# Kernel optimization log

Hardware: AMD Instinct MI355X
Metric: run time of the kernel (lower is better)

## Reference

```python
import jax, jax.numpy as jnp
import numpy as np

N = 4096          # residues (2 chains x 2048)
CHAINS = 2
LMAX = 2
L = (LMAX + 1) ** 2            # 9 spherical coefficients
BBC = 32                       # bb_channels
NBB = 3                        # n_bb_atoms - 1
SPH = BBC + NBB                # 35 sphere channels fed to attention
KNN = 20
LRK = 40
HEADS = 8
HC = 32
VC = HC // 4                   # attn_value_channels = 8
EDGE_F = 32                    # 16 RBF + 16 positional
L_IDX = np.repeat(np.arange(LMAX + 1), 2 * np.arange(LMAX + 1) + 1)  # degree of each of the 9 coeffs


def so3_linear(x, w, b):
    # x: [N,L,Cin]; w: [LMAX+1,Cin,Cout] shared across m within each degree l; bias only on l=0
    out = jnp.einsum('nlc,lcd->nld', x, w[L_IDX])
    return out.at[:, 0, :].add(b)


def _rbf(d):
    mu = jnp.linspace(0.0, 20.0, 16)
    sigma = 20.0 / 16
    return jnp.exp(-(((d[..., None] - mu) / sigma) ** 2))


def _edge_pos_embed(src, dst):
    d = (src - dst).astype(jnp.float32)
    freq = jnp.exp(jnp.arange(0, 16, 2, dtype=jnp.float32) * (-np.log(10000.0) / 16))
    ang = d[:, None] * freq
    return jnp.concatenate([jnp.cos(ang), jnp.sin(ang)], axis=-1)


def setup_inputs():
    key = jax.random.key(0)
    ks = jax.random.split(key, 16)
    n = lambda i, shp, s=1.0: jax.random.normal(ks[i], shp) * s
    return {
        'X_ca': n(0, (N, 3), 10.0),
        'bb_rel': n(1, (N, NBB, 3)),
        'bb_features': n(2, (N, L, BBC)),
        'batch': jnp.repeat(jnp.arange(CHAINS), N // CHAINS),
        'x_mask': jax.random.uniform(ks[3], (N,)) < 0.02,
        'noising_mask': jax.random.uniform(ks[4], (N,)) < 0.5,
        'attn_w1': n(5, (2 * SPH + EDGE_F, HC), 0.05), 'attn_b1': jnp.zeros((HC,)),
        'attn_w2': n(6, (HC, HEADS), 0.05), 'attn_b2': jnp.zeros((HEADS,)),
        'wv': n(7, (LMAX + 1, SPH, HEADS * VC), 0.05), 'bv': jnp.zeros((HEADS * VC,)),
        'wo': n(8, (LMAX + 1, HEADS * VC, BBC), 0.05), 'bo': jnp.zeros((BBC,)),
        'wg': n(9, (BBC, BBC), 0.05), 'bg': jnp.zeros((BBC,)),
        'wf': n(10, (LMAX + 1, BBC, BBC), 0.05), 'bf': jnp.zeros((BBC,)),
        'w_xca': n(11, (LMAX + 1, BBC, 1), 0.05), 'b_xca': jnp.zeros((1,)),
        'w_gate': n(12, (BBC, 1), 0.05), 'b_gate': jnp.zeros((1,)),
        'w_bb': n(13, (LMAX + 1, BBC, NBB), 0.05), 'b_bb': jnp.zeros((NBB,)),
    }


def reference(X_ca, bb_rel, bb_features, batch, x_mask, noising_mask,
              attn_w1, attn_b1, attn_w2, attn_b2, wv, bv, wo, bo, wg, bg, wf, bf,
              w_xca, b_xca, w_gate, b_gate, w_bb, b_bb):
    Nn = X_ca.shape[0]
    BIG = jnp.float32(1e30)
    # ---- graph construction (knn_graph + sample_inv_cubic_edges) ----
    x2 = jnp.sum(X_ca * X_ca, axis=-1)
    D2 = jnp.maximum(x2[:, None] + x2[None, :] - 2.0 * (X_ca @ X_ca.T), 0.0)  # [N,N]
    same = batch[:, None] == batch[None, :]
    eye = jnp.eye(Nn, dtype=bool)
    mask_pair = x_mask[:, None] | x_mask[None, :]
    invalid = (~same) | eye | mask_pair
    knn_idx = jax.lax.top_k(-jnp.where(invalid, BIG, D2), KNN)[1]   # [N,KNN] sources per target
    # long-range: inverse-cubic distance weights, Gumbel top-k sampling, excluding knn picks
    logits = jnp.where(invalid, -BIG, -1.5 * jnp.log(D2 + 1e-6))
    rows = jnp.arange(Nn)[:, None]
    logits = logits.at[rows, knn_idx].set(-BIG)
    gumb = jax.random.gumbel(jax.random.key(1), (Nn, Nn))
    lr_idx = jax.lax.top_k(logits + gumb, LRK)[1]                   # [N,LRK]
    src = jnp.concatenate([knn_idx.reshape(-1), lr_idx.reshape(-1)])
    dst = jnp.concatenate([jnp.repeat(jnp.arange(Nn), KNN), jnp.repeat(jnp.arange(Nn), LRK)])
    # ---- edge features: RBF(dist) + relative positional embedding ----
    dvec = X_ca[src] - X_ca[dst]
    dist = jnp.linalg.norm(dvec, axis=-1)
    edge_feat = jnp.concatenate([_rbf(dist), _edge_pos_embed(src, dst)], axis=-1)  # [M,32]
    # ---- assemble SO3 node embedding [N,L,35] ----
    node = jnp.zeros((Nn, L, SPH), X_ca.dtype)
    node = node.at[:, :, :BBC].set(bb_features)
    node = node.at[:, 1:4, BBC:].set(jnp.swapaxes(bb_rel, -1, -2))  # l=1 coeffs carry bb_rel
    node = node.at[:, 0, SPH - 1].set(noising_mask.astype(X_ca.dtype))
    # ---- equivariant graph attention (simplified TransBlockV2) ----
    inv = node[:, 0, :]                                             # invariant (l=0) features
    a_in = jnp.concatenate([inv[src], inv[dst], edge_feat], axis=-1)
    h = jax.nn.silu(a_in @ attn_w1 + attn_b1)
    logit = h @ attn_w2 + attn_b2                                   # [M,HEADS]
    mx = jax.ops.segment_max(logit, dst, num_segments=Nn)
    p = jnp.exp(logit - mx[dst])
    Z = jax.ops.segment_sum(p, dst, num_segments=Nn)
    alpha = p / (Z[dst] + 1e-9)                                     # segment softmax per target/head
    v = so3_linear(node, wv, bv)[src].reshape(-1, L, HEADS, VC)     # gather source values
    msg = (v * alpha[:, None, :, None]).reshape(-1, L, HEADS * VC)
    agg = jax.ops.segment_sum(msg, dst, num_segments=Nn)            # scatter to targets
    out = so3_linear(agg, wo, bo)                                   # [N,L,32]
    gate = jax.nn.silu(out[:, 0, :] @ wg + bg)                      # invariant-gated FFN
    out = out + so3_linear(out, wf, bf) * gate[:, None, :]
    # ---- coordinate / backbone updates ----
    upd_x = so3_linear(out, w_xca, b_xca)                           # [N,L,1]
    vec = upd_x[:, 1:4, 0]                                          # l=1 -> 3-vector
    g2 = jax.nn.softplus(out[:, 0, :] @ w_gate + b_gate)            # [N,1]
    new_X = X_ca + jnp.where(noising_mask[:, None], vec * g2, 0.0)
    upd_bb = so3_linear(out, w_bb, b_bb)                            # [N,L,3]
    dbb = jnp.swapaxes(upd_bb[:, 1:4, :], -1, -2)                   # [N,3,3]
    new_bb = bb_rel + jnp.where(noising_mask[:, None, None], dbb, 0.0)
    return new_X, new_bb, out
```

## Files before the change

### kernel.cpp

```cpp
#include <hip/hip_runtime.h>
#include <hip/hip_bf16.h>
#include <stdint.h>

#define NN 4096
#define CS 2048
#define KNN 20
#define LRK 40
#define EPN 60
#define NE (NN*EPN)
#define SPHC 35
#define BBCC 32
#define NHEAD 8
#define HVD 64
#define HCD 32
#define LT 9
#define MAXC 384
#define VMB ((NN*LT)/4)
#define NPB (NN/8)

#define INVAL_D2 0xFFFFFFFEu
#define CONSUMED 0xFFFFFFFFu

__device__ __forceinline__ float bf2f(__hip_bfloat16 x) { return __bfloat162float(x); }
__device__ __forceinline__ float bflo(uint32_t d) { return __uint_as_float(d << 16); }
__device__ __forceinline__ float bfhi(uint32_t d) { return __uint_as_float(d & 0xFFFF0000u); }

__device__ __forceinline__ float fast_exp(float x) {
  return __builtin_amdgcn_exp2f(x * 1.4426950408889634f);
}
__device__ __forceinline__ float fast_cos(float a) {
  float rev = a * 0.15915494309189535f;
  rev = rev - __builtin_rintf(rev);
  return __builtin_amdgcn_cosf(rev);
}
__device__ __forceinline__ float fast_sin(float a) {
  float rev = a * 0.15915494309189535f;
  rev = rev - __builtin_rintf(rev);
  return __builtin_amdgcn_sinf(rev);
}

__device__ __forceinline__ float neglogu_f(int i, int j) {
  uint32_t c = ((uint32_t)(i & 2047) << 12) | (uint32_t)j;
  const uint32_t ks0 = 0u, ks1 = 1u, ks2 = 0x1BD11BDBu;
  uint32_t x0 = c + ks0;
  uint32_t x1 = (c + 0x800000u) + ks1;
#define TF_R(r) { x0 += x1; x1 = (x1 << (r)) | (x1 >> (32 - (r))); x1 ^= x0; }
  TF_R(13) TF_R(15) TF_R(26) TF_R(6)   x0 += ks1; x1 += ks2 + 1u;
  TF_R(17) TF_R(29) TF_R(16) TF_R(24)  x0 += ks2; x1 += ks0 + 2u;
  TF_R(13) TF_R(15) TF_R(26) TF_R(6)   x0 += ks0; x1 += ks1 + 3u;
  TF_R(17) TF_R(29) TF_R(16) TF_R(24)  x0 += ks1; x1 += ks2 + 4u;
  TF_R(13) TF_R(15) TF_R(26) TF_R(6)   x0 += ks2; x1 += ks0 + 5u;
#undef TF_R
  uint32_t b = (i >= 2048) ? x1 : x0;
  float u = __uint_as_float((b >> 9) | 0x3F800000u) - 1.0f;
  u = u + 1.17549435e-38f;
  return -logf(u);
}

__global__ __launch_bounds__(256) void prep_proj_kernel(const float* __restrict__ X,
                                                        const int* __restrict__ batch,
                                                        const int* __restrict__ xmask,
                                                        const int* __restrict__ nmask,
                                                        const float* __restrict__ bbf,
                                                        const float* __restrict__ w1,
                                                        const float* __restrict__ b1,
                                                        float4* __restrict__ Xw,
                                                        uint32_t* __restrict__ bm,
                                                        float* __restrict__ Pn,
                                                        float* __restrict__ Pd) {
#pragma clang fp contract(off)
  int tid = threadIdx.x;
  if (blockIdx.x < NPB) {
    int t = tid & 31;
    int n = blockIdx.x * 8 + (tid >> 5);
    float bv_ = bbf[(size_t)n * (LT*BBCC) + t];
    float an = 0.f, ad = b1[t];
    #pragma unroll 8
    for (int c = 0; c < BBCC; c++) {
      float bc = __shfl(bv_, (tid & 32) + c, 64);
      an = fmaf(bc, w1[c * HCD + t], an);
      ad = fmaf(bc, w1[(SPHC + c) * HCD + t], ad);
    }
    float nm = nmask[n] ? 1.f : 0.f;
    an = fmaf(nm, w1[34 * HCD + t], an);
    ad = fmaf(nm, w1[69 * HCD + t], ad);
    Pn[n * HCD + t] = an;
    Pd[n * HCD + t] = ad;
  } else {
    int n = (blockIdx.x - NPB) * 256 + tid;
    if (n >= NN) return;
    float x = X[n*3+0], y = X[n*3+1], z = X[n*3+2];
    float x2 = (x*x + y*y) + z*z;
    Xw[n] = make_float4(x, y, z, x2);
    bm[n] = ((uint32_t)batch[n] << 1) | (xmask[n] ? 1u : 0u);
  }
}

__device__ __forceinline__ void sel2l(uint32_t* val, uint32_t* hist2,
                                      uint32_t* candk, uint32_t* candp,
                                      uint32_t* sh, int* sel,
                                      int k, int base, int cb, int tid) {
  {
    uint4* h4 = (uint4*)hist2;
    uint4 z; z.x = 0; z.y = 0; z.z = 0; z.w = 0;
    h4[tid] = z; h4[tid + 256] = z;
  }
  if (tid == 0) { sh[2] = 0; sh[3] = 0; }
  __syncthreads();
  #pragma unroll
  for (int q = 0; q < 8; q++) {
    uint32_t key = val[tid + (q << 8)];
    atomicAdd(&hist2[key >> 21], 1u);
  }
  __syncthreads();
  uint32_t h[8], s = 0;
  #pragma unroll
  for (int q = 0; q < 8; q++) { h[q] = hist2[tid*8 + q]; s += h[q]; }
  uint32_t cum = s;
  #pragma unroll
  for (int off = 1; off < 64; off <<= 1) {
    uint32_t o = __shfl_up(cum, off, 64);
    if ((tid & 63) >= off) cum += o;
  }
  if ((tid & 63) == 63) sh[8 + (tid >> 6)] = cum;
  __syncthreads();
  uint32_t woff = 0;
  for (int w = 0; w < (tid >> 6); w++) woff += sh[8 + w];
  uint32_t cumAll = cum + woff;
  uint32_t cumBefore = cumAll - s;
  uint32_t rk = (uint32_t)k;
  if (rk > cumBefore && rk <= cumAll) {
    uint32_t rloc = rk - cumBefore, lp = 0;
    bool done = false;
    #pragma unroll
    for (int q = 0; q < 8; q++) {
      lp += h[q];
      if (!done && rloc <= lp) { sh[0] = (uint32_t)(tid*8 + q); sh[1] = rloc - (lp - h[q]); done = true; }
    }
  }
  __syncthreads();
  const uint32_t B = sh[0], r = sh[1];
  #pragma unroll
  for (int q = 0; q < 8; q++) {
    int pos = tid + (q << 8);
    uint32_t key = val[pos];
    if ((key >> 21) == B) {
      uint32_t idx = atomicAdd(&sh[2], 1u);
      if (idx < MAXC) { candk[idx] = key; candp[idx] = (uint32_t)pos; }
    }
  }
  __syncthreads();
  int m = (int)sh[2]; if (m > MAXC) m = MAXC;
  if (tid < 64) {
    for (int ci = tid; ci < m; ci += 64) {
      unsigned long long k64 = ((unsigned long long)candk[ci] << 32) | candp[ci];
      uint32_t rank = 0;
      for (int j = 0; j < m; j++) {
        unsigned long long o = ((unsigned long long)candk[j] << 32) | candp[j];
        rank += (o < k64) ? 1u : 0u;
      }
      if (rank == r - 1) { sh[0] = candk[ci]; sh[1] = candp[ci]; }
    }
  }
  __syncthreads();
  const uint32_t vstar = sh[0], istar = sh[1];
  #pragma unroll
  for (int q = 0; q < 8; q++) {
    int pos = tid + (q << 8);
    uint32_t key = val[pos];
    if (key < vstar || (key == vstar && (uint32_t)pos <= istar)) {
      uint32_t slot = atomicAdd(&sh[3], 1u);
      sel[base + (int)slot] = cb + pos;
    }
  }
  __syncthreads();
}

__global__ __launch_bounds__(256) void select_vmat_kernel(const float4* __restrict__ Xw,
                                                          const uint32_t* __restrict__ bm,
                                                          int* __restrict__ srcO,
                                                          const float* __restrict__ bbf,
                                                          const float* __restrict__ bbrel,
                                                          const int* __restrict__ nmask,
                                                          const float* __restrict__ wv,
                                                          const float* __restrict__ bv,
                                                          __hip_bfloat16* __restrict__ V) {
#pragma clang fp contract(off)
  const int tid = threadIdx.x;
  if (blockIdx.x >= NN) {
    int row = (blockIdx.x - NN) * 4 + (tid >> 6);
    int d = tid & 63;
    if (row >= NN * LT) return;
    int n = row / LT, l = row % LT;
    int li = (l == 0) ? 0 : (l < 4 ? 1 : 2);
    const float* w = wv + (size_t)li * SPHC * HVD;
    float acc = (l == 0) ? bv[d] : 0.f;
    const float* nb = bbf + (size_t)(n*LT + l) * BBCC;
    for (int c = 0; c < BBCC; c++) acc = fmaf(nb[c], w[c*HVD + d], acc);
    if (l >= 1 && l < 4) {
      for (int b = 0; b < 3; b++)
        acc = fmaf(bbrel[(size_t)(n*3 + b)*3 + (l-1)], w[(32+b)*HVD + d], acc);
    }
    if (l == 0) acc = fmaf(nmask[n] ? 1.f : 0.f, w[34*HVD + d], acc);
    V[(size_t)row * HVD + d] = __float2bfloat16(acc);
    return;
  }
  __shared__ uint32_t val[CS];
  __shared__ uint32_t hist2[2048];
  __shared__ uint32_t candk[MAXC];
  __shared__ uint32_t candp[MAXC];
  __shared__ uint32_t sh[12];
  __shared__ int sel[EPN];
  const int i = blockIdx.x;
  const uint32_t bmi = bm[i];

  if (bmi & 1u) {
    if (tid < KNN) srcO[(size_t)i * EPN + tid] = tid;
    else if (tid < EPN) srcO[(size_t)i * EPN + tid] = tid - KNN;
    return;
  }
  const int cb = (int)(bmi >> 1) * CS;
  const float4 xi = Xw[i];

  #pragma unroll
  for (int q = 0; q < 8; q++) {
    int pos = tid + (q << 8);
    int j = cb + pos;
    float4 xj = Xw[j];
    uint32_t bmj = bm[j];
    bool inval = ((bmj & 1u) != 0u) || (j == i);
    float dot = xi.x*xj.x + xi.y*xj.y + xi.z*xj.z;
    float d2r = (xi.w + xj.w) - 2.0f*dot;
    float d2 = d2r > 0.0f ? d2r : 0.0f;
    val[pos] = inval ? INVAL_D2 : __float_as_uint(d2);
  }
  __syncthreads();

  sel2l(val, hist2, candk, candp, sh, sel, KNN, 0, cb, tid);

  if (tid < KNN) val[sel[tid] - cb] = CONSUMED;
  __syncthreads();

  #pragma unroll
  for (int q = 0; q < 8; q++) {
    int pos = tid + (q << 8);
    uint32_t v = val[pos];
    uint32_t skey;
    if (v >= INVAL_D2) skey = CONSUMED;
    else {
      float d2p = __uint_as_float(v) + 1e-6f;
      float w = d2p * sqrtf(d2p) * neglogu_f(i, cb + pos);
      skey = __float_as_uint(w);
    }
    val[pos] = skey;
  }
  __syncthreads();

  sel2l(val, hist2, candk, candp, sh, sel, LRK, KNN, cb, tid);

  if (tid < EPN) srcO[(size_t)i * EPN + tid] = sel[tid];
}

__global__ __launch_bounds__(256) void edge_kernel(const int* __restrict__ src,
                                                   const float4* __restrict__ Xw,
                                                   const float* __restrict__ Pn,
                                                   const float* __restrict__ Pd,
                                                   const float* __restrict__ w1,
                                                   const float* __restrict__ w2,
                                                   const float* __restrict__ b2,
                                                   float* __restrict__ logitO) {
  const float FR[8] = {1.0f, 0.31622776601683794f, 0.1f, 0.031622776601683794f,
                       0.01f, 0.0031622776601683794f, 0.001f, 0.00031622776601683794f};
  __shared__ float w1cf[BBCC][HCD];
  __shared__ float w2f[HCD][NHEAD];
  __shared__ float b2f[NHEAD];
  __shared__ float ef[8][BBCC];
  __shared__ float hbuf[8][HCD];
  int tid = threadIdx.x;
  for (int q = tid; q < BBCC*HCD; q += 256) w1cf[q >> 5][q & 31] = w1[70*HCD + q];
  if (tid < HCD*NHEAD) w2f[tid >> 3][tid & 7] = w2[tid];
  if (tid < NHEAD) b2f[tid] = b2[tid];
  int sub = tid >> 5, t = tid & 31;
  int e = blockIdx.x * 8 + sub;
  int d = e / EPN;
  int s = src[e];
  float4 xs = Xw[s], xd = Xw[d];
  float dx = xs.x - xd.x, dy = xs.y - xd.y, dz = xs.z - xd.z;
  float dist = sqrtf(dx*dx + dy*dy + dz*dz);
  if (t < 16) {
    float mu = (20.0f / 15.0f) * (float)t;
    float zz = (dist - mu) / 1.25f;
    ef[sub][t] = fast_exp(-zz * zz);
  } else {
    int k = t - 16;
    float del = (float)(s - d);
    float a = del * FR[k & 7];
    ef[sub][t] = (k < 8) ? fast_cos(a) : fast_sin(a);
  }
  __syncthreads();
  float a = Pn[s * HCD + t] + Pd[d * HCD + t];
  #pragma unroll
  for (int k = 0; k < BBCC; k++) a = fmaf(ef[sub][k], w1cf[k][t], a);
  hbuf[sub][t] = a / (1.f + fast_exp(-a));
  __syncthreads();
  if (tid < 64) {
    int e2 = tid >> 3, hh = tid & 7;
    float lg = b2f[hh];
    #pragma unroll
    for (int c = 0; c < HCD; c++) lg = fmaf(hbuf[e2][c], w2f[c][hh], lg);
    logitO[(size_t)(blockIdx.x * 8 + e2) * NHEAD + hh] = lg;
  }
}

__global__ __launch_bounds__(256) void node_kernel(const int* __restrict__ src,
                                                  const float* __restrict__ logit,
                                                  const __hip_bfloat16* __restrict__ V,
                                                  const float* __restrict__ wo,
                                                  const float* __restrict__ bo,
                                                  const float* __restrict__ wg,
                                                  const float* __restrict__ bg,
                                                  const float* __restrict__ wf,
                                                  const float* __restrict__ bfb,
                                                  const float* __restrict__ w_xca,
                                                  const float* __restrict__ w_gate,
                                                  const float* __restrict__ b_gate,
                                                  const float* __restrict__ w_bb,
                                                  const float* __restrict__ X,
                                                  const float* __restrict__ bbrel,
                                                  const int* __restrict__ nmask,
                                                  float* __restrict__ out) {
  const int n = blockIdx.x, t = threadIdx.x;
  __shared__ float alpha[EPN][NHEAD];
  __shared__ int slist[EPN];
  __shared__ float aggp[4][LT][HVD];
  __shared__ float agg[LT][HVD];
  __shared__ float o0[LT][BBCC];
  __shared__ float ofin[LT][BBCC];
  __shared__ float gate[BBCC];
  if (t < EPN) slist[t] = src[(size_t)n * EPN + t];
  for (int idx = t; idx < EPN * NHEAD; idx += 256)
    alpha[idx >> 3][idx & 7] = logit[(size_t)n * 480 + idx];
  __syncthreads();
  if (t < NHEAD) {
    float m = -1e30f;
    for (int e = 0; e < EPN; e++) m = fmaxf(m, alpha[e][t]);
    float Z = 0.f;
    for (int e = 0; e < EPN; e++) { float p = expf(alpha[e][t] - m); alpha[e][t] = p; Z += p; }
    float iz = 1.f / (Z + 1e-9f);
    for (int e = 0; e < EPN; e++) alpha[e][t] *= iz;
  }
  __syncthreads();
  {
    const int wave = t >> 6, lane = t & 63;
    const int hM = lane & 7;
    const int hT = (lane & 31) >> 2;
    float accm[8];
    #pragma unroll
    for (int j = 0; j < 8; j++) accm[j] = 0.f;
    float acct0 = 0.f, acct1 = 0.f;
    const int e0 = wave * 15;
    #pragma unroll 5
    for (int e = e0; e < e0 + 15; e++) {
      const uint32_t* Vr = (const uint32_t*)(V + (size_t)slist[e] * (LT * HVD));
      uint4 m = ((const uint4*)Vr)[lane];
      uint32_t tl = (lane < 32) ? Vr[256 + lane] : 0u;
      float am = alpha[e][hM];
      float at = alpha[e][hT];
      accm[0] = fmaf(am, bflo(m.x), accm[0]);
      accm[1] = fmaf(am, bfhi(m.x), accm[1]);
      accm[2] = fmaf(am, bflo(m.y), accm[2]);
      accm[3] = fmaf(am, bfhi(m.y), accm[3]);
      accm[4] = fmaf(am, bflo(m.z), accm[4]);
      accm[5] = fmaf(am, bfhi(m.z), accm[5]);
      accm[6] = fmaf(am, bflo(m.w), accm[6]);
      accm[7] = fmaf(am, bfhi(m.w), accm[7]);
      acct0 = fmaf(at, bflo(tl), acct0);
      acct1 = fmaf(at, bfhi(tl), acct1);
    }
    const int l = lane >> 3, c0 = (lane & 7) * 8;
    #pragma unroll
    for (int j = 0; j < 8; j++) aggp[wave][l][c0 + j] = accm[j];
    if (lane < 32) {
      aggp[wave][8][2*lane]     = acct0;
      aggp[wave][8][2*lane + 1] = acct1;
    }
  }
  __syncthreads();
  for (int idx = t; idx < LT * HVD; idx += 256) {
    int l = idx >> 6, c = idx & 63;
    agg[l][c] = (aggp[0][l][c] + aggp[1][l][c]) + (aggp[2][l][c] + aggp[3][l][c]);
  }
  __syncthreads();
  for (int idx = t; idx < LT * BBCC; idx += 256) {
    int l = idx >> 5, d = idx & 31;
    int li = (l == 0) ? 0 : (l < 4 ? 1 : 2);
    float a = (l == 0) ? bo[d] : 0.f;
    const float* w = wo + (size_t)li * HVD * BBCC;
    for (int c = 0; c < HVD; c++) a = fmaf(agg[l][c], w[c * BBCC + d], a);
    o0[l][d] = a;
  }
  __syncthreads();
  if (t < BBCC) {
    float a = bg[t];
    for (int c = 0; c < BBCC; c++) a = fmaf(o0[0][c], wg[c * BBCC + t], a);
    gate[t] = a / (1.f + expf(-a));
  }
  __syncthreads();
  for (int idx = t; idx < LT * BBCC; idx += 256) {
    int l = idx >> 5, d = idx & 31;
    int li = (l == 0) ? 0 : (l < 4 ? 1 : 2);
    float a = (l == 0) ? bfb[d] : 0.f;
    const float* w = wf + (size_t)li * BBCC * BBCC;
    for (int c = 0; c < BBCC; c++) a = fmaf(o0[l][c], w[c * BBCC + d], a);
    float r = o0[l][d] + a * gate[d];
    ofin[l][d] = r;
    out[49152 + (size_t)n * 288 + idx] = r;
  }
  __syncthreads();
  if (t < 16) {
    float a2 = b_gate[0];
    for (int c = 0; c < BBCC; c++) a2 = fmaf(ofin[0][c], w_gate[c], a2);
    float g2 = fmaxf(a2, 0.f) + log1pf(expf(-fabsf(a2)));
    bool noise = nmask[n] != 0;
    if (t < 3) {
      float a = 0.f;
      for (int d2 = 0; d2 < BBCC; d2++) a = fmaf(ofin[1 + t][d2], w_xca[32 + d2], a);
      float nx = X[n * 3 + t] + (noise ? a * g2 : 0.f);
      out[(size_t)n * 3 + t] = nx;
    }
    if (t < 9) {
      int b = t / 3, c = t % 3;
      float a = 0.f;
      for (int d2 = 0; d2 < BBCC; d2++) a = fmaf(ofin[1 + c][d2], w_bb[(32 + d2) * 3 + b], a);
      float nb = bbrel[(size_t)(n * 3 + b) * 3 + c] + (noise ? a : 0.f);
      out[12288 + (size_t)n * 9 + b * 3 + c] = nb;
    }
  }
}

extern "C" void kernel_launch(void* const* d_in, const int* in_sizes, int n_in,
                              void* d_out, int out_size, void* d_ws, size_t ws_size,
                              hipStream_t stream) {
  (void)in_sizes; (void)n_in; (void)out_size;
  const float* X      = (const float*)d_in[0];
  const float* bbrel  = (const float*)d_in[1];
  const float* bbf    = (const float*)d_in[2];
  const int* batch    = (const int*)d_in[3];
  const int* xmask    = (const int*)d_in[4];
  const int* nmask    = (const int*)d_in[5];
  const float* w1     = (const float*)d_in[6];
  const float* b1     = (const float*)d_in[7];
  const float* w2     = (const float*)d_in[8];
  const float* b2     = (const float*)d_in[9];
  const float* wv     = (const float*)d_in[10];
  const float* bv     = (const float*)d_in[11];
  const float* wo     = (const float*)d_in[12];
  const float* bo     = (const float*)d_in[13];
  const float* wg     = (const float*)d_in[14];
  const float* bg     = (const float*)d_in[15];
  const float* wf     = (const float*)d_in[16];
  const float* bfb    = (const float*)d_in[17];
  const float* w_xca  = (const float*)d_in[18];
  const float* w_gate = (const float*)d_in[20];
  const float* b_gate = (const float*)d_in[21];
  const float* w_bb   = (const float*)d_in[22];

  if (ws_size < 18939904) return;
  char* ws = (char*)d_ws;
  uint32_t* bmp   = (uint32_t*)(ws + 0);
  int*      srcl  = (int*)(ws + 16384);
  float*    logit = (float*)(ws + 999424);
  __hip_bfloat16* V = (__hip_bfloat16*)(ws + 8863744);
  float*    Pn    = (float*)(ws + 13582336);
  float*    Pd    = (float*)(ws + 14106624);
  float4*   Xw    = (float4*)(ws + 14630912);
  float*    out   = (float*)d_out;

  prep_proj_kernel<<<NPB + 16, 256, 0, stream>>>(X, batch, xmask, nmask, bbf, w1, b1,
                                                 Xw, bmp, Pn, Pd);
  select_vmat_kernel<<<NN + VMB, 256, 0, stream>>>(Xw, bmp, srcl, bbf, bbrel, nmask,
                                                   wv, bv, V);
  edge_kernel<<<NE / 8, 256, 0, stream>>>(srcl, Xw, Pn, Pd, w1, w2, b2, logit);
  node_kernel<<<NN, 256, 0, stream>>>(srcl, logit, V, wo, bo, wg, bg, wf, bfb,
                                      w_xca, w_gate, b_gate, w_bb, X, bbrel, nmask, out);
}
```

Before: 273.3 us.

## Fuse edge logit computation into node kernel and merge prep into graph kernel

Four launches become two. Edge MLP logits are now computed per target node inside node_kernel, with edge features passed through wave shuffles, so the logit buffer is no longer written to and read back from global memory. The prep work (Pn/Pd projection, plus the Xw/bm packing) is folded into the selection/V kernel, and coordinates and masks are read directly from the inputs. The trade-off is a longer serial edge phase in each node block (8 iterations, some with idle half-waves) and per-edge data now recomputed per node.

```diff
diff --git a/kernel.cpp b/kernel.cpp
--- a/kernel.cpp
+++ b/kernel.cpp
@@ -7,7 +7,6 @@
 #define KNN 20
 #define LRK 40
 #define EPN 60
-#define NE (NN*EPN)
 #define SPHC 35
 #define BBCC 32
 #define NHEAD 8
@@ -21,7 +20,6 @@
 #define INVAL_D2 0xFFFFFFFEu
 #define CONSUMED 0xFFFFFFFFu
 
-__device__ __forceinline__ float bf2f(__hip_bfloat16 x) { return __bfloat162float(x); }
 __device__ __forceinline__ float bflo(uint32_t d) { return __uint_as_float(d << 16); }
 __device__ __forceinline__ float bfhi(uint32_t d) { return __uint_as_float(d & 0xFFFF0000u); }
 
@@ -57,45 +55,6 @@
   return -logf(u);
 }
 
-__global__ __launch_bounds__(256) void prep_proj_kernel(const float* __restrict__ X,
-                                                        const int* __restrict__ batch,
-                                                        const int* __restrict__ xmask,
-                                                        const int* __restrict__ nmask,
-                                                        const float* __restrict__ bbf,
-                                                        const float* __restrict__ w1,
-                                                        const float* __restrict__ b1,
-                                                        float4* __restrict__ Xw,
-                                                        uint32_t* __restrict__ bm,
-                                                        float* __restrict__ Pn,
-                                                        float* __restrict__ Pd) {
-#pragma clang fp contract(off)
-  int tid = threadIdx.x;
-  if (blockIdx.x < NPB) {
-    int t = tid & 31;
-    int n = blockIdx.x * 8 + (tid >> 5);
-    float bv_ = bbf[(size_t)n * (LT*BBCC) + t];
-    float an = 0.f, ad = b1[t];
-    #pragma unroll 8
-    for (int c = 0; c < BBCC; c++) {
-      float bc = __shfl(bv_, (tid & 32) + c, 64);
-      an = fmaf(bc, w1[c * HCD + t], an);
-      ad = fmaf(bc, w1[(SPHC + c) * HCD + t], ad);
-    }
-    float nm = nmask[n] ? 1.f : 0.f;
-    an = fmaf(nm, w1[34 * HCD + t], an);
-    ad = fmaf(nm, w1[69 * HCD + t], ad);
-    Pn[n * HCD + t] = an;
-    Pd[n * HCD + t] = ad;
-  } else {
-    int n = (blockIdx.x - NPB) * 256 + tid;
-    if (n >= NN) return;
-    float x = X[n*3+0], y = X[n*3+1], z = X[n*3+2];
-    float x2 = (x*x + y*y) + z*z;
-    Xw[n] = make_float4(x, y, z, x2);
-    bm[n] = ((uint32_t)batch[n] << 1) | (xmask[n] ? 1u : 0u);
-  }
-}
-
 __device__ __forceinline__ void sel2l(uint32_t* val, uint32_t* hist2,
                                       uint32_t* candk, uint32_t* candp,
                                       uint32_t* sh, int* sel,
@@ -176,21 +135,43 @@
   __syncthreads();
 }
 
-__global__ __launch_bounds__(256) void select_vmat_kernel(const float4* __restrict__ Xw,
-                                                          const uint32_t* __restrict__ bm,
-                                                          int* __restrict__ srcO,
-                                                          const float* __restrict__ bbf,
-                                                          const float* __restrict__ bbrel,
-                                                          const int* __restrict__ nmask,
-                                                          const float* __restrict__ wv,
-                                                          const float* __restrict__ bv,
-                                                          __hip_bfloat16* __restrict__ V) {
+__global__ __launch_bounds__(256) void graph_kernel(const float* __restrict__ X,
+                                                    const int* __restrict__ batch,
+                                                    const int* __restrict__ xmask,
+                                                    const int* __restrict__ nmask,
+                                                    const float* __restrict__ bbf,
+                                                    const float* __restrict__ bbrel,
+                                                    const float* __restrict__ wv,
+                                                    const float* __restrict__ bv,
+                                                    const float* __restrict__ w1,
+                                                    const float* __restrict__ b1,
+                                                    int* __restrict__ srcO,
+                                                    __hip_bfloat16* __restrict__ V,
+                                                    float* __restrict__ Pn,
+                                                    float* __restrict__ Pd) {
 #pragma clang fp contract(off)
   const int tid = threadIdx.x;
+  if (blockIdx.x >= NN + VMB) {
+    int t = tid & 31;
+    int n = (blockIdx.x - NN - VMB) * 8 + (tid >> 5);
+    float bv_ = bbf[(size_t)n * (LT*BBCC) + t];
+    float an = 0.f, ad = b1[t];
+    #pragma unroll 8
+    for (int c = 0; c < BBCC; c++) {
+      float bc = __shfl(bv_, (tid & 32) + c, 64);
+      an = fmaf(bc, w1[c * HCD + t], an);
+      ad = fmaf(bc, w1[(SPHC + c) * HCD + t], ad);
+    }
+    float nm = nmask[n] ? 1.f : 0.f;
+    an = fmaf(nm, w1[34 * HCD + t], an);
+    ad = fmaf(nm, w1[69 * HCD + t], ad);
+    Pn[n * HCD + t] = an;
+    Pd[n * HCD + t] = ad;
+    return;
+  }
   if (blockIdx.x >= NN) {
     int row = (blockIdx.x - NN) * 4 + (tid >> 6);
     int d = tid & 63;
-    if (row >= NN * LT) return;
     int n = row / LT, l = row % LT;
     int li = (l == 0) ? 0 : (l < 4 ? 1 : 2);
     const float* w = wv + (size_t)li * SPHC * HVD;
@@ -212,25 +193,25 @@
   __shared__ uint32_t sh[12];
   __shared__ int sel[EPN];
   const int i = blockIdx.x;
-  const uint32_t bmi = bm[i];
-
-  if (bmi & 1u) {
+
+  if (xmask[i]) {
     if (tid < KNN) srcO[(size_t)i * EPN + tid] = tid;
     else if (tid < EPN) srcO[(size_t)i * EPN + tid] = tid - KNN;
     return;
   }
-  const int cb = (int)(bmi >> 1) * CS;
-  const float4 xi = Xw[i];
+  const int cb = batch[i] * CS;
+  const float xi0 = X[i*3+0], xi1 = X[i*3+1], xi2 = X[i*3+2];
+  const float x2i = (xi0*xi0 + xi1*xi1) + xi2*xi2;
 
   #pragma unroll
   for (int q = 0; q < 8; q++) {
     int pos = tid + (q << 8);
     int j = cb + pos;
-    float4 xj = Xw[j];
-    uint32_t bmj = bm[j];
-    bool inval = ((bmj & 1u) != 0u) || (j == i);
-    float dot = xi.x*xj.x + xi.y*xj.y + xi.z*xj.z;
-    float d2r = (xi.w + xj.w) - 2.0f*dot;
+    float xj0 = X[j*3+0], xj1 = X[j*3+1], xj2 = X[j*3+2];
+    float x2j = (xj0*xj0 + xj1*xj1) + xj2*xj2;
+    bool inval = (xmask[j] != 0) || (j == i);
+    float dot = xi0*xj0 + xi1*xj1 + xi2*xj2;
+    float d2r = (x2i + x2j) - 2.0f*dot;
     float d2 = d2r > 0.0f ? d2r : 0.0f;
     val[pos] = inval ? INVAL_D2 : __float_as_uint(d2);
   }
@@ -261,60 +242,13 @@
   if (tid < EPN) srcO[(size_t)i * EPN + tid] = sel[tid];
 }
 
-__global__ __launch_bounds__(256) void edge_kernel(const int* __restrict__ src,
-                                                   const float4* __restrict__ Xw,
-                                                   const float* __restrict__ Pn,
-                                                   const float* __restrict__ Pd,
-                                                   const float* __restrict__ w1,
-                                                   const float* __restrict__ w2,
-                                                   const float* __restrict__ b2,
-                                                   float* __restrict__ logitO) {
-  const float FR[8] = {1.0f, 0.31622776601683794f, 0.1f, 0.031622776601683794f,
-                       0.01f, 0.0031622776601683794f, 0.001f, 0.00031622776601683794f};
-  __shared__ float w1cf[BBCC][HCD];
-  __shared__ float w2f[HCD][NHEAD];
-  __shared__ float b2f[NHEAD];
-  __shared__ float ef[8][BBCC];
-  __shared__ float hbuf[8][HCD];
-  int tid = threadIdx.x;
-  for (int q = tid; q < BBCC*HCD; q += 256) w1cf[q >> 5][q & 31] = w1[70*HCD + q];
-  if (tid < HCD*NHEAD) w2f[tid >> 3][tid & 7] = w2[tid];
-  if (tid < NHEAD) b2f[tid] = b2[tid];
-  int sub = tid >> 5, t = tid & 31;
-  int e = blockIdx.x * 8 + sub;
-  int d = e / EPN;
-  int s = src[e];
-  float4 xs = Xw[s], xd = Xw[d];
-  float dx = xs.x - xd.x, dy = xs.y - xd.y, dz = xs.z - xd.z;
-  float dist = sqrtf(dx*dx + dy*dy + dz*dz);
-  if (t < 16) {
-    float mu = (20.0f / 15.0f) * (float)t;
-    float zz = (dist - mu) / 1.25f;
-    ef[sub][t] = fast_exp(-zz * zz);
-  } else {
-    int k = t - 16;
-    float del = (float)(s - d);
-    float a = del * FR[k & 7];
-    ef[sub][t] = (k < 8) ? fast_cos(a) : fast_sin(a);
-  }
-  __syncthreads();
-  float a = Pn[s * HCD + t] + Pd[d * HCD + t];
-  #pragma unroll
-  for (int k = 0; k < BBCC; k++) a = fmaf(ef[sub][k], w1cf[k][t], a);
-  hbuf[sub][t] = a / (1.f + fast_exp(-a));
-  __syncthreads();
-  if (tid < 64) {
-    int e2 = tid >> 3, hh = tid & 7;
-    float lg = b2f[hh];
-    #pragma unroll
-    for (int c = 0; c < HCD; c++) lg = fmaf(hbuf[e2][c], w2f[c][hh], lg);
-    logitO[(size_t)(blockIdx.x * 8 + e2) * NHEAD + hh] = lg;
-  }
-}
-
 __global__ __launch_bounds__(256) void node_kernel(const int* __restrict__ src,
-                                                  const float* __restrict__ logit,
                                                   const __hip_bfloat16* __restrict__ V,
+                                                  const float* __restrict__ Pn,
+                                                  const float* __restrict__ Pd,
+                                                  const float* __restrict__ w1,
+                                                  const float* __restrict__ w2,
+                                                  const float* __restrict__ b2,
                                                   const float* __restrict__ wo,
                                                   const float* __restrict__ bo,
                                                   const float* __restrict__ wg,
@@ -329,17 +263,66 @@
                                                   const float* __restrict__ bbrel,
                                                   const int* __restrict__ nmask,
                                                   float* __restrict__ out) {
+  const float FR[8] = {1.0f, 0.31622776601683794f, 0.1f, 0.031622776601683794f,
+                       0.01f, 0.0031622776601683794f, 0.001f, 0.00031622776601683794f};
   const int n = blockIdx.x, t = threadIdx.x;
   __shared__ float alpha[EPN][NHEAD];
   __shared__ int slist[EPN];
+  __shared__ float w1cf[BBCC][HCD];
+  __shared__ float w2f[HCD][NHEAD];
+  __shared__ float b2f[NHEAD];
+  __shared__ float hb[4][2][HCD];
   __shared__ float aggp[4][LT][HVD];
   __shared__ float agg[LT][HVD];
   __shared__ float o0[LT][BBCC];
   __shared__ float ofin[LT][BBCC];
   __shared__ float gate[BBCC];
   if (t < EPN) slist[t] = src[(size_t)n * EPN + t];
-  for (int idx = t; idx < EPN * NHEAD; idx += 256)
-    alpha[idx >> 3][idx & 7] = logit[(size_t)n * 480 + idx];
+  for (int q = t; q < BBCC*HCD; q += 256) w1cf[q >> 5][q & 31] = w1[70*HCD + q];
+  if (t < HCD*NHEAD) w2f[t >> 3][t & 7] = w2[t];
+  if (t < NHEAD) b2f[t] = b2[t];
+  __syncthreads();
+  {
+    const int w = t >> 6, lane = t & 63, sub = (t >> 5) & 1, tl = t & 31;
+    const float xn0 = X[n*3+0], xn1 = X[n*3+1], xn2 = X[n*3+2];
+    const float pdn = Pd[n * HCD + tl];
+    const int e0 = w * 15;
+    for (int q = 0; q < 8; q++) {
+      int el = 2*q + sub;
+      bool valid = el < 15;
+      int e = e0 + el;
+      float efv = 0.f;
+      int s = 0;
+      if (valid) {
+        s = slist[e];
+        if (tl < 16) {
+          float dx = X[s*3+0] - xn0, dy = X[s*3+1] - xn1, dz = X[s*3+2] - xn2;
+          float dist = sqrtf(dx*dx + dy*dy + dz*dz);
+          float mu = (20.0f / 15.0f) * (float)tl;
+          float zz = (dist - mu) / 1.25f;
+          efv = fast_exp(-zz * zz);
+        } else {
+          int k = tl - 16;
+          float del = (float)(s - n);
+          float a = del * FR[k & 7];
+          efv = (k < 8) ? fast_cos(a) : fast_sin(a);
+        }
+      }
+      if (valid) {
+        float a = Pn[s * HCD + tl] + pdn;
+        #pragma unroll
+        for (int k = 0; k < BBCC; k++)
+          a = fmaf(__shfl(efv, (lane & 32) + k, 64), w1cf[k][tl], a);
+        hb[w][sub][tl] = a / (1.f + fast_exp(-a));
+      }
+      if (valid && tl < NHEAD) {
+        float lg = b2f[tl];
+        #pragma unroll
+        for (int c = 0; c < HCD; c++) lg = fmaf(hb[w][sub][c], w2f[c][tl], lg);
+        alpha[e][tl] = lg;
+      }
+    }
+  }
   __syncthreads();
   if (t < NHEAD) {
     float m = -1e30f;
@@ -363,7 +346,7 @@
     for (int e = e0; e < e0 + 15; e++) {
       const uint32_t* Vr = (const uint32_t*)(V + (size_t)slist[e] * (LT * HVD));
       uint4 m = ((const uint4*)Vr)[lane];
-      uint32_t tl = (lane < 32) ? Vr[256 + lane] : 0u;
+      uint32_t tl2 = (lane < 32) ? Vr[256 + lane] : 0u;
       float am = alpha[e][hM];
       float at = alpha[e][hT];
       accm[0] = fmaf(am, bflo(m.x), accm[0]);
@@ -374,8 +357,8 @@
       accm[5] = fmaf(am, bfhi(m.z), accm[5]);
       accm[6] = fmaf(am, bflo(m.w), accm[6]);
       accm[7] = fmaf(am, bfhi(m.w), accm[7]);
-      acct0 = fmaf(at, bflo(tl), acct0);
-      acct1 = fmaf(at, bfhi(tl), acct1);
+      acct0 = fmaf(at, bflo(tl2), acct0);
+      acct1 = fmaf(at, bfhi(tl2), acct1);
     }
     const int l = lane >> 3, c0 = (lane & 7) * 8;
     #pragma unroll
@@ -467,20 +450,16 @@
 
   if (ws_size < 18939904) return;
   char* ws = (char*)d_ws;
-  uint32_t* bmp   = (uint32_t*)(ws + 0);
-  int*      srcl  = (int*)(ws + 16384);
-  float*    logit = (float*)(ws + 999424);
-  __hip_bfloat16* V = (__hip_bfloat16*)(ws + 8863744);
-  float*    Pn    = (float*)(ws + 13582336);
-  float*    Pd    = (float*)(ws + 14106624);
-  float4*   Xw    = (float4*)(ws + 14630912);
+  int*      srcl  = (int*)(ws + 0);
+  __hip_bfloat16* V = (__hip_bfloat16*)(ws + 983040);
+  float*    Pn    = (float*)(ws + 5701632);
+  float*    Pd    = (float*)(ws + 6225920);
   float*    out   = (float*)d_out;
 
-  prep_proj_kernel<<<NPB + 16, 256, 0, stream>>>(X, batch, xmask, nmask, bbf, w1, b1,
-                                                 Xw, bmp, Pn, Pd);
-  select_vmat_kernel<<<NN + VMB, 256, 0, stream>>>(Xw, bmp, srcl, bbf, bbrel, nmask,
-                                                   wv, bv, V);
-  edge_kernel<<<NE / 8, 256, 0, stream>>>(srcl, Xw, Pn, Pd, w1, w2, b2, logit);
-  node_kernel<<<NN, 256, 0, stream>>>(srcl, logit, V, wo, bo, wg, bg, wf, bfb,
-                                      w_xca, w_gate, b_gate, w_bb, X, bbrel, nmask, out);
-}
+  graph_kernel<<<NN + VMB + NPB, 256, 0, stream>>>(X, batch, xmask, nmask, bbf, bbrel,
+                                                   wv, bv, w1, b1, srcl, V, Pn, Pd);
+  node_kernel<<<NN, 256, 0, stream>>>(srcl, V, Pn, Pd, w1, w2, b2,
+                                      wo, bo, wg, bg, wf, bfb,
+                                      w_xca, w_gate, b_gate, w_bb,
+                                      X, bbrel, nmask, out);
+}
```

Result: slower. 283.7 us (+3.8%).
